# Kernel optimization log

Hardware: AMD Instinct MI355X
Metric: run time of the kernel (lower is better)

Reference implementation:

```python
import jax, jax.numpy as jnp
import numpy as np
from jax import lax

EPS = 1e-08


def setup_inputs() -> dict:
    key = jax.random.key(0)
    k1, k2, k3 = jax.random.split(key, 3)
    B, Cin, Cout, K, H, W = 8, 512, 512, 3, 64, 64
    feature_map = jax.random.normal(k1, (B, Cin, H, W), dtype=jnp.float32)
    style = jax.random.normal(k2, (B, Cin), dtype=jnp.float32)
    weight = jax.random.normal(k3, (Cout, Cin, K, K), dtype=jnp.float32)
    return {"feature_map": feature_map, "style": style, "weight": weight}


def reference(feature_map, style, weight):
    # EqualizedWeight: scale raw N(0,1) weight by 1/sqrt(fan_in)
    Cout, Cin, K, _ = weight.shape
    gain = 1.0 / np.sqrt(Cin * K * K)
    w = weight * gain  # (O, I, K, K)

    # Modulate: per-sample scale of input channels -> (B, O, I, K, K)
    w = w[None] * style[:, None, :, None, None]

    # Demodulate: normalize each (b, o) filter to unit norm
    sigma_inv = lax.rsqrt(jnp.sum(w * w, axis=(2, 3, 4), keepdims=True) + EPS)
    w = w * sigma_inv

    # Per-sample conv2d, padding 'same' (equivalent to the groups=B trick)
    def conv_one(x, wi):  # x: (I, H, W), wi: (O, I, K, K)
        return lax.conv_general_dilated(
            x[None], wi, window_strides=(1, 1), padding="SAME",
            dimension_numbers=("NCHW", "OIHW", "NCHW"))[0]

    return jax.vmap(conv_one)(feature_map, w)  # (B, O, H, W)
```

## Files before the change

### kernel.cpp

```cpp
#include <hip/hip_runtime.h>

typedef unsigned short u16;
typedef __attribute__((ext_vector_type(8))) short s16x8;
typedef __attribute__((ext_vector_type(4))) float floatx4;

#define XT_ROWELEMS 2112
#define XT_CGELEMS  139392
#define XT_PB       4460544ull
#define WM_ELEMS    2359296ull
#define WM_PB       4718592ull

#define GLDS(gp, lp) __builtin_amdgcn_global_load_lds(                      \
    (const __attribute__((address_space(1))) void*)(gp),                    \
    (__attribute__((address_space(3))) void*)(lp), 16, 0, 0)

__device__ __forceinline__ u16 f2bf(float f) {
  union { float f; unsigned u; } x; x.f = f;
  unsigned r = x.u + 0x7fffu + ((x.u >> 16) & 1u);
  return (u16)(r >> 16);
}

__device__ __forceinline__ void transpose_unit(
    char* smraw, const float* __restrict__ fm, u16* __restrict__ xt, int ti, int tid)
{
  u16* sm16 = (u16*)smraw;
  const int y = ti & 63, cgi = (ti >> 6) & 15, bl = ti >> 10;
  const float* src = fm + (((size_t)bl * 512 + cgi * 32) * 64 + y) * 64;
  const int x4 = (tid & 15) * 4;
#pragma unroll
  for (int it = 0; it < 2; ++it) {
    int ci = (tid >> 4) + it * 16;
    float4 v = *(const float4*)&src[(size_t)ci * 4096 + x4];
    sm16[(x4 + 0) * 40 + ci] = f2bf(v.x);
    sm16[(x4 + 1) * 40 + ci] = f2bf(v.y);
    sm16[(x4 + 2) * 40 + ci] = f2bf(v.z);
    sm16[(x4 + 3) * 40 + ci] = f2bf(v.w);
  }

  u16* cgbase = xt + (size_t)(bl * 16 + cgi) * XT_CGELEMS;
  const uint4 z = {0u, 0u, 0u, 0u};
  u16* rowb = cgbase + (size_t)(y + 1) * XT_ROWELEMS;
  if (tid < 4)              ((uint4*)rowb)[tid] = z;
  else if (tid < 8)         ((uint4*)(rowb + 65 * 32))[tid - 4] = z;
  if (y == 0)  for (int i = tid; i < 264; i += 256) ((uint4*)cgbase)[i] = z;
  if (y == 63) for (int i = tid; i < 264; i += 256) ((uint4*)(cgbase + 65 * XT_ROWELEMS))[i] = z;

  __syncthreads();
  const int x = tid >> 2;
  uint4 u = *(const uint4*)&sm16[x * 40 + (tid & 3) * 8];
  const int col = 1 + x;
  const int slot = (tid & 3) ^ ((col >> 1) & 3);
  ((uint4*)rowb)[col * 4 + slot] = u;
}

__device__ __forceinline__ void modulate_unit(
    char* smraw, const float* __restrict__ w, const float* __restrict__ style,
    u16* __restrict__ wm, int mi, int tid)
{
  float* sv = (float*)smraw;
  float* red = (float*)(smraw + 18432);
  const int o = mi & 511, bl = mi >> 9;
  const float gain = 0.014731391f;
  const float* wo = w + (size_t)o * 4608;
  const float* st = style + (size_t)bl * 512;
  float ss = 0.f;
#pragma unroll
  for (int j = 0; j < 5; ++j) {
    int s4 = j * 256 + tid;
    if (s4 < 1152) {
      float4 v = *(const float4*)&wo[s4 * 4];
      int i0 = s4 * 4;
      int c0 = i0 / 9, rem = i0 - c0 * 9;
      float sa = st[c0];
      float sb = st[c0 < 511 ? c0 + 1 : 511];
      float w0 = v.x * gain * sa;
      float w1 = v.y * gain * (rem + 1 >= 9 ? sb : sa);
      float w2 = v.z * gain * (rem + 2 >= 9 ? sb : sa);
      float w3 = v.w * gain * (rem + 3 >= 9 ? sb : sa);
      floatx4 wv = {w0, w1, w2, w3};
      ((floatx4*)sv)[s4] = wv;
      ss += w0 * w0 + w1 * w1 + w2 * w2 + w3 * w3;
    }
  }
#pragma unroll
  for (int off = 32; off > 0; off >>= 1) ss += __shfl_down(ss, off, 64);
  if ((tid & 63) == 0) red[tid >> 6] = ss;
  __syncthreads();
  float sinv = rsqrtf(red[0] + red[1] + red[2] + red[3] + 1e-8f);
  const int axor = ((o >> 1) & 3) << 3;
  u16* base = wm + (size_t)bl * WM_ELEMS + (size_t)o * 32;
  const int c0 = tid * 2;
  const int pos = (c0 & 31) ^ axor;
#pragma unroll
  for (int t = 0; t < 9; ++t) {
    unsigned lo = f2bf(sv[c0 * 9 + t] * sinv);
    unsigned hi = f2bf(sv[(c0 + 1) * 9 + t] * sinv);
    *(unsigned*)(base + ((size_t)(t * 16 + (c0 >> 5))) * 16384 + pos) = lo | (hi << 16);
  }
}

__global__ __launch_bounds__(256) void prep_fused(
    const float* __restrict__ fm, const float* __restrict__ w,
    const float* __restrict__ style, u16* __restrict__ xt,
    u16* __restrict__ wm, int b0)
{
  __shared__ __align__(16) char smraw[18448];
  const int bid = blockIdx.x;
  const int g = bid / 3, rrole = bid - g * 3;
  const int tid = threadIdx.x;
  if (rrole < 2) {
    const int ti0 = g * 2 + rrole;
    const int y = ti0 & 63, cgi = (ti0 >> 6) & 15, bl = ti0 >> 10;
    transpose_unit(smraw, fm + (size_t)b0 * 512 * 4096,
                   xt, (bl << 10) | (cgi << 6) | y, tid);
  } else {
    const int o = g & 511, bl = g >> 9;
    modulate_unit(smraw, w, style + (size_t)b0 * 512, wm, (bl << 9) | o, tid);
  }
}

__global__ __launch_bounds__(128, 2) void conv_mfma(
    const u16* __restrict__ Wmod, const u16* __restrict__ xt,
    float* __restrict__ out, int b0, int nb)
{
  const int id = blockIdx.x;
  const int bl = id % nb;
  const int rest = id / nb;
  const int og = rest & 3, p_blk = rest >> 2;
  const int tid = threadIdx.x;
  const int lane = tid & 63, wave = tid >> 6;
  const int wn_off = wave * 64;
  const int l15 = lane & 15, quad = lane >> 4;

  __shared__ __align__(16) u16 As[2][4096];
  __shared__ __align__(16) u16 Bs[8448];

  const int y0 = p_blk * 2;
  const size_t xt_base = ((size_t)(bl * 16) * XT_CGELEMS) + (size_t)y0 * XT_ROWELEMS;
  const size_t w_base = (size_t)bl * WM_ELEMS + (size_t)og * (128 * 32);

  auto stage_b = [&](int cgi) {
    const char* g = (const char*)(xt + xt_base + (size_t)cgi * XT_CGELEMS);
    for (int r = wave; r < 16; r += 2)
      GLDS(g + r * 1024 + lane * 16, (char*)Bs + r * 1024);
    if (wave == 0 && lane < 32)
      GLDS(g + 16384 + lane * 16, (char*)Bs + 16384);
  };
  auto stage_a = [&](int t, int cgi, int buf) {
    const char* g = (const char*)(Wmod + w_base + (size_t)(t * 16 + cgi) * 16384);
    for (int r = wave; r < 8; r += 2)
      GLDS(g + r * 1024 + lane * 16, (char*)As[buf] + r * 1024);
  };

  int aoff[8];
#pragma unroll
  for (int mt = 0; mt < 8; ++mt) {
    int row = mt * 16 + l15;
    aoff[mt] = row * 32 + ((quad ^ ((row >> 1) & 3)) << 3);
  }
  int pr[4], pc[4];
#pragma unroll
  for (int nt = 0; nt < 4; ++nt) {
    int p = wn_off + nt * 16 + l15;
    pr[nt] = p >> 6; pc[nt] = p & 63;
  }

  floatx4 acc[8][4];
  const floatx4 zf = {0.f, 0.f, 0.f, 0.f};
#pragma unroll
  for (int mt = 0; mt < 8; ++mt)
#pragma unroll
    for (int nt = 0; nt < 4; ++nt) acc[mt][nt] = zf;

  stage_b(0);
  stage_a(0, 0, 0);
  __syncthreads();

#pragma unroll 1
  for (int cgi = 0; cgi < 16; ++cgi) {
#pragma unroll 1
    for (int t = 0; t < 9; ++t) {
      const int cur = (cgi * 9 + t) & 1, nxt = cur ^ 1;
      const bool last = (cgi == 15 && t == 8);
      const bool cgb = (t == 8 && cgi < 15);
      if (!last) stage_a(t < 8 ? t + 1 : 0, t < 8 ? cgi : cgi + 1, nxt);

      const int ky = t / 3, kx = t - ky * 3;
      s16x8 afr[8], bfr[4];
      const u16* Ab = As[cur];
#pragma unroll
      for (int nt = 0; nt < 4; ++nt) {
        int r = pr[nt] + ky, c = pc[nt] + kx;
        bfr[nt] = *(const s16x8*)&Bs[(r * 66 + c) * 32 + ((quad ^ ((c >> 1) & 3)) << 3)];
      }
#pragma unroll
      for (int mt = 0; mt < 8; ++mt)
        afr[mt] = *(const s16x8*)&Ab[aoff[mt]];
#pragma unroll
      for (int mt = 0; mt < 8; ++mt)
#pragma unroll
        for (int nt = 0; nt < 4; ++nt)
          acc[mt][nt] = __builtin_amdgcn_mfma_f32_16x16x32_bf16(
              afr[mt], bfr[nt], acc[mt][nt], 0, 0, 0);

      if (cgb) {
        __syncthreads();
        stage_b(cgi + 1);
      }
      __syncthreads();
    }
  }

  float* outp = out + ((size_t)(b0 + bl) * 512 + og * 128) * 4096 + p_blk * 128;
#pragma unroll
  for (int mt = 0; mt < 8; ++mt)
#pragma unroll
    for (int nt = 0; nt < 4; ++nt) {
      int n = wn_off + nt * 16 + l15;
#pragma unroll
      for (int r = 0; r < 4; ++r) {
        int m = mt * 16 + quad * 4 + r;
        outp[(size_t)m * 4096 + n] = acc[mt][nt][r];
      }
    }
}

__global__ __launch_bounds__(256) void conv_direct(
    const float* __restrict__ fm, const float* __restrict__ style,
    const float* __restrict__ w, float* __restrict__ out)
{
  const int o = blockIdx.x, b = blockIdx.y, tid = threadIdx.x;
  __shared__ float swm[4608];
  __shared__ float red[4];
  const float gain = 0.014731391f;
  const float* wo = w + (size_t)o * 4608;
  const float* st = style + (size_t)b * 512;
  float ss = 0.f;
#pragma unroll
  for (int j = 0; j < 18; ++j) {
    int idx = j * 256 + tid;
    float v = wo[idx] * gain * st[idx / 9];
    swm[idx] = v;
    ss += v * v;
  }
#pragma unroll
  for (int off = 32; off > 0; off >>= 1) ss += __shfl_down(ss, off, 64);
  if ((tid & 63) == 0) red[tid >> 6] = ss;
  __syncthreads();
  const float sinv = rsqrtf(red[0] + red[1] + red[2] + red[3] + 1e-8f);

  const int y = tid >> 2, x0 = (tid & 3) * 16;
  float acc[16];
#pragma unroll
  for (int i = 0; i < 16; ++i) acc[i] = 0.f;
  const float* fb = fm + (size_t)b * 512 * 4096;
  for (int ci = 0; ci < 512; ++ci) {
    const float* fc = fb + (size_t)ci * 4096;
    const float* wr = swm + ci * 9;
#pragma unroll
    for (int ky = 0; ky < 3; ++ky) {
      int yy = y + ky - 1;
      if (yy < 0 || yy > 63) continue;
      const float* frow = fc + yy * 64;
#pragma unroll
      for (int kx = 0; kx < 3; ++kx) {
        float wv = wr[ky * 3 + kx];
#pragma unroll
        for (int i = 0; i < 16; ++i) {
          int xx = x0 + i + kx - 1;
          float xv = (xx >= 0 && xx < 64) ? frow[xx] : 0.f;
          acc[i] += wv * xv;
        }
      }
    }
  }
  float* op = out + ((size_t)b * 512 + o) * 4096 + y * 64 + x0;
#pragma unroll
  for (int i = 0; i < 16; ++i) op[i] = acc[i] * sinv;
}

extern "C" void kernel_launch(void* const* d_in, const int* in_sizes, int n_in,
                              void* d_out, int out_size, void* d_ws, size_t ws_size,
                              hipStream_t stream) {
  const float* fm = (const float*)d_in[0];
  const float* style = (const float*)d_in[1];
  const float* w = (const float*)d_in[2];
  float* out = (float*)d_out;

  if (ws_size < XT_PB + WM_PB) {
    conv_direct<<<dim3(512, 8), 256, 0, stream>>>(fm, style, w, out);
    return;
  }
  int nb = 8;
  while (nb > 1 && (size_t)nb * (XT_PB + WM_PB) > ws_size) nb >>= 1;

  u16* xt = (u16*)d_ws;
  u16* wmod = (u16*)((char*)d_ws + (size_t)nb * XT_PB);

  for (int b0 = 0; b0 < 8; b0 += nb) {
    prep_fused<<<dim3(1536 * nb), 256, 0, stream>>>(fm, w, style, xt, wmod, b0);
    conv_mfma<<<dim3(128 * nb), 128, 0, stream>>>(wmod, xt, out, b0, nb);
  }
}
```

Baseline: 271.8 us.

## Load modulated weights directly into registers and double-buffer input tile in LDS

Weight fragments for the MFMA A operand now come straight from global memory into registers, split into two halves so the next step's first half is prefetched while the second half computes. The LDS weight buffers and the per-step barrier are removed. The input tile is double-buffered and the next channel group is staged once per group. Weights are written unswizzled to match the new direct-load pattern. This trades LDS traffic and barriers for more global/L2 load latency exposed on each step and higher register pressure.

```diff
diff --git a/kernel.cpp b/kernel.cpp
--- a/kernel.cpp
+++ b/kernel.cpp
@@ -87,10 +87,9 @@
   if ((tid & 63) == 0) red[tid >> 6] = ss;
   __syncthreads();
   float sinv = rsqrtf(red[0] + red[1] + red[2] + red[3] + 1e-8f);
-  const int axor = ((o >> 1) & 3) << 3;
   u16* base = wm + (size_t)bl * WM_ELEMS + (size_t)o * 32;
   const int c0 = tid * 2;
-  const int pos = (c0 & 31) ^ axor;
+  const int pos = c0 & 31;
 #pragma unroll
   for (int t = 0; t < 9; ++t) {
     unsigned lo = f2bf(sv[c0 * 9 + t] * sinv);
@@ -132,32 +131,21 @@
   const int wn_off = wave * 64;
   const int l15 = lane & 15, quad = lane >> 4;
 
-  __shared__ __align__(16) u16 As[2][4096];
-  __shared__ __align__(16) u16 Bs[8448];
+  __shared__ __align__(16) u16 Bs[2][8448];
 
   const int y0 = p_blk * 2;
   const size_t xt_base = ((size_t)(bl * 16) * XT_CGELEMS) + (size_t)y0 * XT_ROWELEMS;
-  const size_t w_base = (size_t)bl * WM_ELEMS + (size_t)og * (128 * 32);
-
-  auto stage_b = [&](int cgi) {
+  const u16* aP = Wmod + (size_t)bl * WM_ELEMS + og * 4096 + l15 * 32 + quad * 8;
+
+  auto stage_b = [&](int cgi, int half) {
     const char* g = (const char*)(xt + xt_base + (size_t)cgi * XT_CGELEMS);
+    char* l = (char*)Bs[half];
     for (int r = wave; r < 16; r += 2)
-      GLDS(g + r * 1024 + lane * 16, (char*)Bs + r * 1024);
+      GLDS(g + r * 1024 + lane * 16, l + r * 1024);
     if (wave == 0 && lane < 32)
-      GLDS(g + 16384 + lane * 16, (char*)Bs + 16384);
+      GLDS(g + 16384 + lane * 16, l + 16384);
   };
-  auto stage_a = [&](int t, int cgi, int buf) {
-    const char* g = (const char*)(Wmod + w_base + (size_t)(t * 16 + cgi) * 16384);
-    for (int r = wave; r < 8; r += 2)
-      GLDS(g + r * 1024 + lane * 16, (char*)As[buf] + r * 1024);
-  };
-
-  int aoff[8];
-#pragma unroll
-  for (int mt = 0; mt < 8; ++mt) {
-    int row = mt * 16 + l15;
-    aoff[mt] = row * 32 + ((quad ^ ((row >> 1) & 3)) << 3);
-  }
+
   int pr[4], pc[4];
 #pragma unroll
   for (int nt = 0; nt < 4; ++nt) {
@@ -172,42 +160,53 @@
 #pragma unroll
     for (int nt = 0; nt < 4; ++nt) acc[mt][nt] = zf;
 
-  stage_b(0);
-  stage_a(0, 0, 0);
+  s16x8 a03[4];
+#pragma unroll
+  for (int mt = 0; mt < 4; ++mt) a03[mt] = *(const s16x8*)(aP + mt * 512);
+  stage_b(0, 0);
   __syncthreads();
 
 #pragma unroll 1
-  for (int cgi = 0; cgi < 16; ++cgi) {
+  for (int cg = 0; cg < 16; ++cg) {
+    if (cg) __syncthreads();
+    const u16* Bc = Bs[cg & 1];
 #pragma unroll 1
     for (int t = 0; t < 9; ++t) {
-      const int cur = (cgi * 9 + t) & 1, nxt = cur ^ 1;
-      const bool last = (cgi == 15 && t == 8);
-      const bool cgb = (t == 8 && cgi < 15);
-      if (!last) stage_a(t < 8 ? t + 1 : 0, t < 8 ? cgi : cgi + 1, nxt);
+      const u16* pS = aP + (size_t)(t * 16 + cg) * 16384;
+      s16x8 a47[4];
+#pragma unroll
+      for (int mt = 0; mt < 4; ++mt)
+        a47[mt] = *(const s16x8*)(pS + (mt + 4) * 512);
+      if (t == 0 && cg < 15) stage_b(cg + 1, (cg + 1) & 1);
 
       const int ky = t / 3, kx = t - ky * 3;
-      s16x8 afr[8], bfr[4];
-      const u16* Ab = As[cur];
+      s16x8 bfr[4];
 #pragma unroll
       for (int nt = 0; nt < 4; ++nt) {
         int r = pr[nt] + ky, c = pc[nt] + kx;
-        bfr[nt] = *(const s16x8*)&Bs[(r * 66 + c) * 32 + ((quad ^ ((c >> 1) & 3)) << 3)];
+        bfr[nt] = *(const s16x8*)&Bc[(r * 66 + c) * 32 + ((quad ^ ((c >> 1) & 3)) << 3)];
       }
 #pragma unroll
-      for (int mt = 0; mt < 8; ++mt)
-        afr[mt] = *(const s16x8*)&Ab[aoff[mt]];
-#pragma unroll
-      for (int mt = 0; mt < 8; ++mt)
+      for (int mt = 0; mt < 4; ++mt)
 #pragma unroll
         for (int nt = 0; nt < 4; ++nt)
           acc[mt][nt] = __builtin_amdgcn_mfma_f32_16x16x32_bf16(
-              afr[mt], bfr[nt], acc[mt][nt], 0, 0, 0);
-
-      if (cgb) {
-        __syncthreads();
-        stage_b(cgi + 1);
+              a03[mt], bfr[nt], acc[mt][nt], 0, 0, 0);
+
+      if (!(cg == 15 && t == 8)) {
+        const int tn = (t == 8) ? 0 : t + 1;
+        const int cgn = (t == 8) ? cg + 1 : cg;
+        const u16* pN = aP + (size_t)(tn * 16 + cgn) * 16384;
+#pragma unroll
+        for (int mt = 0; mt < 4; ++mt)
+          a03[mt] = *(const s16x8*)(pN + mt * 512);
       }
-      __syncthreads();
+#pragma unroll
+      for (int mt = 0; mt < 4; ++mt)
+#pragma unroll
+        for (int nt = 0; nt < 4; ++nt)
+          acc[mt + 4][nt] = __builtin_amdgcn_mfma_f32_16x16x32_bf16(
+              a47[mt], bfr[nt], acc[mt + 4][nt], 0, 0, 0);
     }
   }
 
```

New measurement: 275.9 us. Within noise of the previous version (+1.5%).

## Switch conv GEMM to 32x32x16 MFMA with 256-channel block tiles

Applied to the files above, without the earlier changes.

Each block now covers 256 output channels and 128 pixels using 4 waves (2x2) instead of 128 channels with 2 waves, and the inner product uses 32x32x16 bf16 MFMA instead of 16x16x32. The B tile in LDS is reused across twice as many output channels, and the larger MFMA shape needs fewer LDS fragment loads per FLOP. In exchange the grid is halved to 512 blocks, which may hurt load balance across CUs, and LDS per block grows, which can lower occupancy.

```diff
diff --git a/kernel.cpp b/kernel.cpp
--- a/kernel.cpp
+++ b/kernel.cpp
@@ -3,6 +3,7 @@
 typedef unsigned short u16;
 typedef __attribute__((ext_vector_type(8))) short s16x8;
 typedef __attribute__((ext_vector_type(4))) float floatx4;
+typedef __attribute__((ext_vector_type(16))) float floatx16;
 
 #define XT_ROWELEMS 2112
 #define XT_CGELEMS  139392
@@ -119,58 +120,61 @@
   }
 }
 
-__global__ __launch_bounds__(128, 2) void conv_mfma(
+__global__ __launch_bounds__(256, 2) void conv_mfma(
     const u16* __restrict__ Wmod, const u16* __restrict__ xt,
     float* __restrict__ out, int b0, int nb)
 {
   const int id = blockIdx.x;
   const int bl = id % nb;
   const int rest = id / nb;
-  const int og = rest & 3, p_blk = rest >> 2;
+  const int og = rest & 1, p_blk = rest >> 1;
   const int tid = threadIdx.x;
   const int lane = tid & 63, wave = tid >> 6;
-  const int wn_off = wave * 64;
-  const int l15 = lane & 15, quad = lane >> 4;
-
-  __shared__ __align__(16) u16 As[2][4096];
+  const int wm_off = (wave & 1) * 128, wn_off = (wave >> 1) * 64;
+  const int l31 = lane & 31, h = lane >> 5;
+
+  __shared__ __align__(16) u16 As[2][8192];
   __shared__ __align__(16) u16 Bs[8448];
 
   const int y0 = p_blk * 2;
   const size_t xt_base = ((size_t)(bl * 16) * XT_CGELEMS) + (size_t)y0 * XT_ROWELEMS;
-  const size_t w_base = (size_t)bl * WM_ELEMS + (size_t)og * (128 * 32);
+  const size_t w_base = (size_t)bl * WM_ELEMS + (size_t)og * (256 * 32);
 
   auto stage_b = [&](int cgi) {
     const char* g = (const char*)(xt + xt_base + (size_t)cgi * XT_CGELEMS);
-    for (int r = wave; r < 16; r += 2)
+    for (int r = wave; r < 16; r += 4)
       GLDS(g + r * 1024 + lane * 16, (char*)Bs + r * 1024);
     if (wave == 0 && lane < 32)
       GLDS(g + 16384 + lane * 16, (char*)Bs + 16384);
   };
   auto stage_a = [&](int t, int cgi, int buf) {
     const char* g = (const char*)(Wmod + w_base + (size_t)(t * 16 + cgi) * 16384);
-    for (int r = wave; r < 8; r += 2)
+    for (int r = wave; r < 16; r += 4)
       GLDS(g + r * 1024 + lane * 16, (char*)As[buf] + r * 1024);
   };
 
-  int aoff[8];
-#pragma unroll
-  for (int mt = 0; mt < 8; ++mt) {
-    int row = mt * 16 + l15;
-    aoff[mt] = row * 32 + ((quad ^ ((row >> 1) & 3)) << 3);
-  }
-  int pr[4], pc[4];
-#pragma unroll
-  for (int nt = 0; nt < 4; ++nt) {
-    int p = wn_off + nt * 16 + l15;
+  int aoff[4][2];
+#pragma unroll
+  for (int mt = 0; mt < 4; ++mt) {
+    int row = wm_off + mt * 32 + l31;
+#pragma unroll
+    for (int kh = 0; kh < 2; ++kh)
+      aoff[mt][kh] = row * 32 + (((kh * 2 + h) ^ ((row >> 1) & 3)) << 3);
+  }
+  int pr[2], pc[2];
+#pragma unroll
+  for (int nt = 0; nt < 2; ++nt) {
+    int p = wn_off + nt * 32 + l31;
     pr[nt] = p >> 6; pc[nt] = p & 63;
   }
 
-  floatx4 acc[8][4];
-  const floatx4 zf = {0.f, 0.f, 0.f, 0.f};
-#pragma unroll
-  for (int mt = 0; mt < 8; ++mt)
-#pragma unroll
-    for (int nt = 0; nt < 4; ++nt) acc[mt][nt] = zf;
+  floatx16 acc[4][2];
+#pragma unroll
+  for (int mt = 0; mt < 4; ++mt)
+#pragma unroll
+    for (int nt = 0; nt < 2; ++nt)
+#pragma unroll
+      for (int r = 0; r < 16; ++r) acc[mt][nt][r] = 0.f;
 
   stage_b(0);
   stage_a(0, 0, 0);
@@ -186,22 +190,26 @@
       if (!last) stage_a(t < 8 ? t + 1 : 0, t < 8 ? cgi : cgi + 1, nxt);
 
       const int ky = t / 3, kx = t - ky * 3;
-      s16x8 afr[8], bfr[4];
       const u16* Ab = As[cur];
 #pragma unroll
-      for (int nt = 0; nt < 4; ++nt) {
-        int r = pr[nt] + ky, c = pc[nt] + kx;
-        bfr[nt] = *(const s16x8*)&Bs[(r * 66 + c) * 32 + ((quad ^ ((c >> 1) & 3)) << 3)];
+      for (int kh = 0; kh < 2; ++kh) {
+        s16x8 afr[4], bfr[2];
+#pragma unroll
+        for (int nt = 0; nt < 2; ++nt) {
+          int r = pr[nt] + ky, c = pc[nt] + kx;
+          bfr[nt] = *(const s16x8*)&Bs[(r * 66 + c) * 32 +
+                                       (((kh * 2 + h) ^ ((c >> 1) & 3)) << 3)];
+        }
+#pragma unroll
+        for (int mt = 0; mt < 4; ++mt)
+          afr[mt] = *(const s16x8*)&Ab[aoff[mt][kh]];
+#pragma unroll
+        for (int mt = 0; mt < 4; ++mt)
+#pragma unroll
+          for (int nt = 0; nt < 2; ++nt)
+            acc[mt][nt] = __builtin_amdgcn_mfma_f32_32x32x16_bf16(
+                afr[mt], bfr[nt], acc[mt][nt], 0, 0, 0);
       }
-#pragma unroll
-      for (int mt = 0; mt < 8; ++mt)
-        afr[mt] = *(const s16x8*)&Ab[aoff[mt]];
-#pragma unroll
-      for (int mt = 0; mt < 8; ++mt)
-#pragma unroll
-        for (int nt = 0; nt < 4; ++nt)
-          acc[mt][nt] = __builtin_amdgcn_mfma_f32_16x16x32_bf16(
-              afr[mt], bfr[nt], acc[mt][nt], 0, 0, 0);
 
       if (cgb) {
         __syncthreads();
@@ -211,15 +219,15 @@
     }
   }
 
-  float* outp = out + ((size_t)(b0 + bl) * 512 + og * 128) * 4096 + p_blk * 128;
-#pragma unroll
-  for (int mt = 0; mt < 8; ++mt)
-#pragma unroll
-    for (int nt = 0; nt < 4; ++nt) {
-      int n = wn_off + nt * 16 + l15;
-#pragma unroll
-      for (int r = 0; r < 4; ++r) {
-        int m = mt * 16 + quad * 4 + r;
+  float* outp = out + ((size_t)(b0 + bl) * 512 + og * 256) * 4096 + p_blk * 128;
+#pragma unroll
+  for (int mt = 0; mt < 4; ++mt)
+#pragma unroll
+    for (int nt = 0; nt < 2; ++nt) {
+      int n = wn_off + nt * 32 + l31;
+#pragma unroll
+      for (int r = 0; r < 16; ++r) {
+        int m = wm_off + mt * 32 + (r & 3) + 8 * (r >> 2) + 4 * h;
         outp[(size_t)m * 4096 + n] = acc[mt][nt][r];
       }
     }
@@ -299,6 +307,6 @@
 
   for (int b0 = 0; b0 < 8; b0 += nb) {
     prep_fused<<<dim3(1536 * nb), 256, 0, stream>>>(fm, w, style, xt, wmod, b0);
-    conv_mfma<<<dim3(128 * nb), 128, 0, stream>>>(wmod, xt, out, b0, nb);
-  }
-}
+    conv_mfma<<<dim3(64 * nb), 256, 0, stream>>>(wmod, xt, out, b0, nb);
+  }
+}
```

After: 277.5 us. 1.02x slower.

## Enlarge conv MFMA block tile to 256 channels with triple-buffered weight staging

Applied to the files above, without the earlier changes.

Each conv block now computes 256 output channels with 4 waves (a 2x2 wave grid) instead of 128 channels with 2 waves. This halves the grid and doubles reuse of each staged input tile. Weight tiles are triple-buffered and prefetched two steps ahead. Full __syncthreads are replaced by explicit vmcnt waits plus raw barriers, and the tap loop is unrolled. The goal is to cut redundant input loads and barrier stalls, at the cost of more LDS per block (about 66KB) and a single wave of 512 blocks, which may leave occupancy imbalanced.

```diff
diff --git a/kernel.cpp b/kernel.cpp
--- a/kernel.cpp
+++ b/kernel.cpp
@@ -13,6 +13,8 @@
 #define GLDS(gp, lp) __builtin_amdgcn_global_load_lds(                      \
     (const __attribute__((address_space(1))) void*)(gp),                    \
     (__attribute__((address_space(3))) void*)(lp), 16, 0, 0)
+
+#define WAITVM(N) asm volatile("s_waitcnt vmcnt(" #N ")" ::: "memory")
 
 __device__ __forceinline__ u16 f2bf(float f) {
   union { float f; unsigned u; } x; x.f = f;
@@ -119,43 +121,43 @@
   }
 }
 
-__global__ __launch_bounds__(128, 2) void conv_mfma(
+__global__ __launch_bounds__(256, 2) void conv_mfma(
     const u16* __restrict__ Wmod, const u16* __restrict__ xt,
     float* __restrict__ out, int b0, int nb)
 {
   const int id = blockIdx.x;
   const int bl = id % nb;
   const int rest = id / nb;
-  const int og = rest & 3, p_blk = rest >> 2;
+  const int og = rest & 1, p_blk = rest >> 1;
   const int tid = threadIdx.x;
   const int lane = tid & 63, wave = tid >> 6;
-  const int wn_off = wave * 64;
+  const int wm_off = (wave & 1) * 128, wn_off = (wave >> 1) * 64;
   const int l15 = lane & 15, quad = lane >> 4;
 
-  __shared__ __align__(16) u16 As[2][4096];
+  __shared__ __align__(16) u16 As[3][8192];
   __shared__ __align__(16) u16 Bs[8448];
 
   const int y0 = p_blk * 2;
   const size_t xt_base = ((size_t)(bl * 16) * XT_CGELEMS) + (size_t)y0 * XT_ROWELEMS;
-  const size_t w_base = (size_t)bl * WM_ELEMS + (size_t)og * (128 * 32);
+  const size_t w_base = (size_t)bl * WM_ELEMS + (size_t)og * (256 * 32);
 
   auto stage_b = [&](int cgi) {
     const char* g = (const char*)(xt + xt_base + (size_t)cgi * XT_CGELEMS);
-    for (int r = wave; r < 16; r += 2)
+    for (int r = wave; r < 16; r += 4)
       GLDS(g + r * 1024 + lane * 16, (char*)Bs + r * 1024);
     if (wave == 0 && lane < 32)
       GLDS(g + 16384 + lane * 16, (char*)Bs + 16384);
   };
   auto stage_a = [&](int t, int cgi, int buf) {
     const char* g = (const char*)(Wmod + w_base + (size_t)(t * 16 + cgi) * 16384);
-    for (int r = wave; r < 8; r += 2)
+    for (int r = wave; r < 16; r += 4)
       GLDS(g + r * 1024 + lane * 16, (char*)As[buf] + r * 1024);
   };
 
   int aoff[8];
 #pragma unroll
   for (int mt = 0; mt < 8; ++mt) {
-    int row = mt * 16 + l15;
+    int row = wm_off + mt * 16 + l15;
     aoff[mt] = row * 32 + ((quad ^ ((row >> 1) & 3)) << 3);
   }
   int pr[4], pc[4];
@@ -174,16 +176,28 @@
 
   stage_b(0);
   stage_a(0, 0, 0);
-  __syncthreads();
+  stage_a(1, 0, 1);
+  WAITVM(4);
+  __builtin_amdgcn_s_barrier();
+  __builtin_amdgcn_sched_barrier(0);
 
 #pragma unroll 1
   for (int cgi = 0; cgi < 16; ++cgi) {
-#pragma unroll 1
+#pragma unroll
     for (int t = 0; t < 9; ++t) {
-      const int cur = (cgi * 9 + t) & 1, nxt = cur ^ 1;
-      const bool last = (cgi == 15 && t == 8);
-      const bool cgb = (t == 8 && cgi < 15);
-      if (!last) stage_a(t < 8 ? t + 1 : 0, t < 8 ? cgi : cgi + 1, nxt);
+      const int s = cgi * 9 + t;
+      const int cur = t % 3;
+      if (s > 0) {
+        if (t == 0 || s == 1 || s == 143) { WAITVM(0); }
+        else                              { WAITVM(4); }
+        __builtin_amdgcn_s_barrier();
+        __builtin_amdgcn_sched_barrier(0);
+      }
+      if (s + 2 <= 143) {
+        int t2 = t + 2, cg2 = cgi;
+        if (t2 >= 9) { t2 -= 9; ++cg2; }
+        stage_a(t2, cg2, (t + 2) % 3);
+      }
 
       const int ky = t / 3, kx = t - ky * 3;
       s16x8 afr[8], bfr[4];
@@ -203,15 +217,15 @@
           acc[mt][nt] = __builtin_amdgcn_mfma_f32_16x16x32_bf16(
               afr[mt], bfr[nt], acc[mt][nt], 0, 0, 0);
 
-      if (cgb) {
-        __syncthreads();
+      if (t == 8 && cgi < 15) {
+        __builtin_amdgcn_s_barrier();
+        __builtin_amdgcn_sched_barrier(0);
         stage_b(cgi + 1);
       }
-      __syncthreads();
     }
   }
 
-  float* outp = out + ((size_t)(b0 + bl) * 512 + og * 128) * 4096 + p_blk * 128;
+  float* outp = out + ((size_t)(b0 + bl) * 512 + og * 256) * 4096 + p_blk * 128;
 #pragma unroll
   for (int mt = 0; mt < 8; ++mt)
 #pragma unroll
@@ -219,7 +233,7 @@
       int n = wn_off + nt * 16 + l15;
 #pragma unroll
       for (int r = 0; r < 4; ++r) {
-        int m = mt * 16 + quad * 4 + r;
+        int m = wm_off + mt * 16 + quad * 4 + r;
         outp[(size_t)m * 4096 + n] = acc[mt][nt][r];
       }
     }
@@ -299,6 +313,6 @@
 
   for (int b0 = 0; b0 < 8; b0 += nb) {
     prep_fused<<<dim3(1536 * nb), 256, 0, stream>>>(fm, w, style, xt, wmod, b0);
-    conv_mfma<<<dim3(128 * nb), 128, 0, stream>>>(wmod, xt, out, b0, nb);
-  }
-}
+    conv_mfma<<<dim3(64 * nb), 256, 0, stream>>>(wmod, xt, out, b0, nb);
+  }
+}
```

After: 268.7 us. About the same (-1.1%).
